# Optimization experiments

Measured on AMD Instinct MI355X. Metric: run time of the kernel, lower is better.

## Reference

```python
import jax, jax.numpy as jnp
import numpy as np

BATCH, TOK, DIM, OUT = 4, 2048, 4096, 4096
E, R, TOP_K = 8, 16, 2
SCALING = 16.0 / R  # lora_alpha / r


def setup_inputs() -> dict:
    key = jax.random.key(0)
    ks = jax.random.split(key, 6)
    return {
        "x": jax.random.normal(ks[0], (BATCH, TOK, DIM), dtype=jnp.float32),
        "W_base": jax.random.normal(ks[1], (OUT, DIM), dtype=jnp.float32) / np.sqrt(DIM),
        "b_base": jax.random.normal(ks[2], (OUT,), dtype=jnp.float32) * 0.01,
        "W_gate": jax.random.normal(ks[3], (E, DIM), dtype=jnp.float32) * 0.01,
        "A": jax.random.normal(ks[4], (E, R, DIM), dtype=jnp.float32) / np.sqrt(DIM),
        "B": jax.random.normal(ks[5], (OUT, OUT // OUT * R * 0 + R), dtype=jnp.float32)[None].repeat(E, 0) * 0.0 + jax.random.normal(ks[5], (E, OUT, R), dtype=jnp.float32) * 0.02,
    }


def reference(x, W_base, b_base, W_gate, A, B):
    # Base frozen linear: [B,N,D] @ [D,O] -> [B,N,O]
    result = jnp.einsum("bnd,od->bno", x, W_base) + b_base
    # Gating
    logits = jnp.einsum("bnd,ed->bne", x, W_gate)
    probs = jax.nn.softmax(logits.astype(jnp.float32), axis=-1)  # fp32 softmax
    top_p, top_i = jax.lax.top_k(probs, TOP_K)  # [B,N,K]
    top_p = top_p / jnp.sum(top_p, axis=-1, keepdims=True)  # top_k > 1 branch
    top_p = top_p.astype(x.dtype)
    # Scatter top-k probs back to dense [B,N,E] routing weights
    route_w = jnp.sum(jax.nn.one_hot(top_i, E, dtype=x.dtype) * top_p[..., None], axis=-2)
    # Per-expert LoRA: down-project all tokens for all experts (r is small),
    # weight by routing, then up-project and sum over experts.
    h = jnp.einsum("bnd,erd->bner", x, A)          # [B,N,E,r]
    hw = h * route_w[..., None]                      # mask/combine weighting
    delta = jnp.einsum("bner,eor->bno", hw, B)      # [B,N,O]
    return result + delta * SCALING
```

## Files before the change

kernel.cpp:

```cpp
#include <hip/hip_runtime.h>
#include <hip/hip_bf16.h>
#include <cstdint>

#define TOKENS 8192
#define DIM_   4096
#define OUTD   4096
#define NE     8
#define NR     16
#define LORA_COLS (NE*NR)
#define KCAT  (DIM_ + LORA_COLS)
#define NTILES (KCAT/64)
#define HSPLIT 8
#define HKC    (DIM_/HSPLIT)

typedef __attribute__((ext_vector_type(8))) short short8;
typedef __attribute__((ext_vector_type(4))) float f32x4;

__device__ __forceinline__ unsigned short f2bf(float f) {
  union { float f; unsigned u; } v; v.f = f;
  unsigned r = v.u + 0x7FFFu + ((v.u >> 16) & 1u);
  return (unsigned short)(r >> 16);
}

__device__ __forceinline__ void load_lds16(const void* g, void* l) {
  auto gp = reinterpret_cast<const __attribute__((address_space(1))) unsigned int*>(
      reinterpret_cast<uintptr_t>(g));
  auto lp = reinterpret_cast<__attribute__((address_space(3))) unsigned int*>(
      reinterpret_cast<uintptr_t>(l));
  __builtin_amdgcn_global_load_lds(gp, lp, 16, 0, 0);
}

#define BAR() asm volatile("s_barrier" ::: "memory")
#define LGKM0() do { asm volatile("s_waitcnt lgkmcnt(0)" ::: "memory"); \
                     __builtin_amdgcn_sched_barrier(0); } while (0)
#define VMW(N) asm volatile("s_waitcnt vmcnt(" #N ")" ::: "memory")

__global__ __launch_bounds__(256) void conv_w_kernel(
    const float* __restrict__ W, const float* __restrict__ Bm,
    const float* __restrict__ Am, unsigned short* __restrict__ Wcat,
    unsigned short* __restrict__ Acat, float scaling) {
  int b = blockIdx.x, tid = threadIdx.x;
  if (b < OUTD) {
    const float4* src = (const float4*)(W + (size_t)b * DIM_);
    unsigned short* dst = Wcat + (size_t)b * KCAT;
#pragma unroll
    for (int j = 0; j < DIM_ / 1024; ++j) {
      float4 v = src[j * 256 + tid];
      ushort4 o; o.x = f2bf(v.x); o.y = f2bf(v.y); o.z = f2bf(v.z); o.w = f2bf(v.w);
      *(ushort4*)(dst + (size_t)(j * 256 + tid) * 4) = o;
    }
    if (tid < LORA_COLS) {
      int e = tid >> 4, r = tid & 15;
      dst[DIM_ + tid] = f2bf(scaling * Bm[((size_t)e * OUTD + b) * NR + r]);
    }
  } else {
    int i = b - OUTD;
    const float4* src = (const float4*)(Am + (size_t)i * DIM_);
    unsigned short* dst = Acat + (size_t)i * DIM_;
#pragma unroll
    for (int j = 0; j < DIM_ / 1024; ++j) {
      float4 v = src[j * 256 + tid];
      ushort4 o; o.x = f2bf(v.x); o.y = f2bf(v.y); o.z = f2bf(v.z); o.w = f2bf(v.w);
      *(ushort4*)(dst + (size_t)(j * 256 + tid) * 4) = o;
    }
  }
}

__global__ __launch_bounds__(256) void prep_x_kernel(
    const float* __restrict__ x, const float* __restrict__ Wg,
    unsigned short* __restrict__ Xcat, int* __restrict__ ridx,
    float* __restrict__ rw) {
  __shared__ float red[32 * 257];
  __shared__ float lg[32];
  int tid = threadIdx.x;
  int t0 = blockIdx.x * 4;
  float acc[4][8];
#pragma unroll
  for (int ti = 0; ti < 4; ++ti)
#pragma unroll
    for (int e = 0; e < 8; ++e) acc[ti][e] = 0.f;
  const float4* x4 = (const float4*)x;
  const float4* wg4 = (const float4*)Wg;
#pragma unroll
  for (int j = 0; j < 4; ++j) {
    int dpos = j * 256 + tid;
    float4 wg[8];
#pragma unroll
    for (int e = 0; e < 8; ++e) wg[e] = wg4[e * 1024 + dpos];
#pragma unroll
    for (int ti = 0; ti < 4; ++ti) {
      float4 v = x4[(size_t)(t0 + ti) * 1024 + dpos];
      ushort4 o; o.x = f2bf(v.x); o.y = f2bf(v.y); o.z = f2bf(v.z); o.w = f2bf(v.w);
      *(ushort4*)&Xcat[(size_t)(t0 + ti) * KCAT + (size_t)dpos * 4] = o;
#pragma unroll
      for (int e = 0; e < 8; ++e)
        acc[ti][e] += v.x * wg[e].x + v.y * wg[e].y + v.z * wg[e].z + v.w * wg[e].w;
    }
  }
#pragma unroll
  for (int p = 0; p < 32; ++p) red[p * 257 + tid] = acc[p >> 3][p & 7];
  __syncthreads();
  {
    int p = tid >> 3, part = tid & 7;
    float s = 0.f;
#pragma unroll
    for (int i = 0; i < 32; ++i) s += red[p * 257 + part * 32 + i];
    s += __shfl_xor(s, 1);
    s += __shfl_xor(s, 2);
    s += __shfl_xor(s, 4);
    if (part == 0) lg[p] = s;
  }
  __syncthreads();
  if (tid < 4) {
    float l[8];
#pragma unroll
    for (int e = 0; e < 8; ++e) l[e] = lg[tid * 8 + e];
    int i0 = 0; float m0 = l[0];
#pragma unroll
    for (int e = 1; e < 8; ++e) if (l[e] > m0) { m0 = l[e]; i0 = e; }
    int i1 = -1; float m1 = -3.4e38f;
#pragma unroll
    for (int e = 0; e < 8; ++e) if (e != i0 && l[e] > m1) { m1 = l[e]; i1 = e; }
    float w0 = 1.0f / (1.0f + expf(m1 - m0));
    int t = t0 + tid;
    ridx[t * 2] = i0; ridx[t * 2 + 1] = i1;
    rw[t * 2] = w0;  rw[t * 2 + 1] = 1.0f - w0;
  }
}

template <int MODE>
__global__ __launch_bounds__(256) void gemm_kernel(
    const unsigned short* __restrict__ Aop, const unsigned short* __restrict__ Bop,
    float* __restrict__ Cout, unsigned short* __restrict__ CoutBf,
    const float* __restrict__ bias, const int* __restrict__ ridx,
    const float* __restrict__ rw,
    int M, int N, int K, int lda, int ldb, int ldc) {
  __shared__ __align__(16) unsigned short lsA[128 * 32];
  __shared__ __align__(16) unsigned short lsB[128 * 32];
  int tid = threadIdx.x;
  int lane = tid & 63, wave = tid >> 6;
  int wm = wave >> 1, wn = wave & 1;
  int row0 = blockIdx.x * 128, col0 = blockIdx.y * 128;

  f32x4 acc[4][4];
#pragma unroll
  for (int a = 0; a < 4; ++a)
#pragma unroll
    for (int b = 0; b < 4; ++b) acc[a][b] = (f32x4){0.f, 0.f, 0.f, 0.f};

  int lrow = lane >> 2;
  int lcol = (lane & 3) << 3;
  int fr = lane & 15, fk = (lane >> 4) << 3;

  const unsigned short* gA0 = Aop + (size_t)(row0 + wave * 32 + lrow) * lda + lcol;
  const unsigned short* gA1 = Aop + (size_t)(row0 + wave * 32 + 16 + lrow) * lda + lcol;
  const unsigned short* gB0 = Bop + (size_t)(col0 + wave * 32 + lrow) * ldb + lcol;
  const unsigned short* gB1 = Bop + (size_t)(col0 + wave * 32 + 16 + lrow) * ldb + lcol;

  for (int k0 = 0; k0 < K; k0 += 32) {
    load_lds16(gA0 + k0, lsA + wave * 1024);
    load_lds16(gA1 + k0, lsA + wave * 1024 + 512);
    load_lds16(gB0 + k0, lsB + wave * 1024);
    load_lds16(gB1 + k0, lsB + wave * 1024 + 512);
    __syncthreads();
    short8 af[4], bfr[4];
#pragma unroll
    for (int mi = 0; mi < 4; ++mi)
      af[mi] = *(const short8*)&lsA[(wm * 64 + mi * 16 + fr) * 32 + fk];
#pragma unroll
    for (int ni = 0; ni < 4; ++ni)
      bfr[ni] = *(const short8*)&lsB[(wn * 64 + ni * 16 + fr) * 32 + fk];
#pragma unroll
    for (int mi = 0; mi < 4; ++mi)
#pragma unroll
      for (int ni = 0; ni < 4; ++ni)
        acc[mi][ni] = __builtin_amdgcn_mfma_f32_16x16x32_bf16(af[mi], bfr[ni], acc[mi][ni], 0, 0, 0);
    __syncthreads();
  }

  int fg = lane >> 4;
  if (MODE == 0) {
#pragma unroll
    for (int ni = 0; ni < 4; ++ni) {
      int col = col0 + wn * 64 + ni * 16 + fr;
      float bv = bias[col];
#pragma unroll
      for (int mi = 0; mi < 4; ++mi)
#pragma unroll
        for (int j = 0; j < 4; ++j) {
          int row = row0 + wm * 64 + mi * 16 + fg * 4 + j;
          Cout[(size_t)row * ldc + col] = acc[mi][ni][j] + bv;
        }
    }
  } else {
#pragma unroll
    for (int mi = 0; mi < 4; ++mi)
#pragma unroll
      for (int j = 0; j < 4; ++j) {
        int row = row0 + wm * 64 + mi * 16 + fg * 4 + j;
        int i0 = ridx[row * 2], i1 = ridx[row * 2 + 1];
        float w0 = rw[row * 2], w1 = rw[row * 2 + 1];
#pragma unroll
        for (int ni = 0; ni < 4; ++ni) {
          int col = wn * 64 + ni * 16 + fr;
          int e = col >> 4;
          float w = (e == i0) ? w0 : ((e == i1) ? w1 : 0.f);
          CoutBf[(size_t)row * ldc + col] = f2bf(w * acc[mi][ni][j]);
        }
      }
  }
}

__global__ __launch_bounds__(256) void gemm_h_sk_kernel(
    const unsigned short* __restrict__ Aop,
    const unsigned short* __restrict__ Bop,
    float* __restrict__ Hpart) {
  __shared__ __align__(16) unsigned short lsA[128 * 32];
  __shared__ __align__(16) unsigned short lsB[128 * 32];
  int tid = threadIdx.x;
  int lane = tid & 63, wave = tid >> 6;
  int wm = wave >> 1, wn = wave & 1;
  int row0 = blockIdx.x * 128;
  int s = blockIdx.y;
  int kbeg = s * HKC;

  f32x4 acc[4][4];
#pragma unroll
  for (int a = 0; a < 4; ++a)
#pragma unroll
    for (int b = 0; b < 4; ++b) acc[a][b] = (f32x4){0.f, 0.f, 0.f, 0.f};

  int lrow = lane >> 2;
  int lcol = (lane & 3) << 3;
  int fr = lane & 15, fk = (lane >> 4) << 3;

  const unsigned short* gA0 = Aop + (size_t)(row0 + wave * 32 + lrow) * KCAT + lcol;
  const unsigned short* gA1 = Aop + (size_t)(row0 + wave * 32 + 16 + lrow) * KCAT + lcol;
  const unsigned short* gB0 = Bop + (size_t)(wave * 32 + lrow) * DIM_ + lcol;
  const unsigned short* gB1 = Bop + (size_t)(wave * 32 + 16 + lrow) * DIM_ + lcol;

  for (int k0 = kbeg; k0 < kbeg + HKC; k0 += 32) {
    load_lds16(gA0 + k0, lsA + wave * 1024);
    load_lds16(gA1 + k0, lsA + wave * 1024 + 512);
    load_lds16(gB0 + k0, lsB + wave * 1024);
    load_lds16(gB1 + k0, lsB + wave * 1024 + 512);
    __syncthreads();
    short8 af[4], bfr[4];
#pragma unroll
    for (int mi = 0; mi < 4; ++mi)
      af[mi] = *(const short8*)&lsA[(wm * 64 + mi * 16 + fr) * 32 + fk];
#pragma unroll
    for (int ni = 0; ni < 4; ++ni)
      bfr[ni] = *(const short8*)&lsB[(wn * 64 + ni * 16 + fr) * 32 + fk];
#pragma unroll
    for (int mi = 0; mi < 4; ++mi)
#pragma unroll
      for (int ni = 0; ni < 4; ++ni)
        acc[mi][ni] = __builtin_amdgcn_mfma_f32_16x16x32_bf16(af[mi], bfr[ni], acc[mi][ni], 0, 0, 0);
    __syncthreads();
  }

  int fg = lane >> 4;
  float* outp = Hpart + (size_t)s * TOKENS * 128;
#pragma unroll
  for (int ni = 0; ni < 4; ++ni) {
    int col = wn * 64 + ni * 16 + fr;
#pragma unroll
    for (int mi = 0; mi < 4; ++mi)
#pragma unroll
      for (int j = 0; j < 4; ++j) {
        int row = row0 + wm * 64 + mi * 16 + fg * 4 + j;
        outp[(size_t)row * 128 + col] = acc[mi][ni][j];
      }
  }
}

__global__ __launch_bounds__(256) void h_combine_kernel(
    const float* __restrict__ Hpart, const int* __restrict__ ridx,
    const float* __restrict__ rw, unsigned short* __restrict__ Xcat) {
  int gid = blockIdx.x * 256 + threadIdx.x;
  int t = gid >> 7, c = gid & 127;
  float s = 0.f;
#pragma unroll
  for (int i = 0; i < HSPLIT; ++i) s += Hpart[(size_t)i * TOKENS * 128 + gid];
  int e = c >> 4;
  int i0 = ridx[t * 2], i1 = ridx[t * 2 + 1];
  float w = (e == i0) ? rw[t * 2] : ((e == i1) ? rw[t * 2 + 1] : 0.f);
  Xcat[(size_t)t * KCAT + DIM_ + c] = f2bf(w * s);
}

#define RD_A4(dst, base, ks, mi0) do { \
  dst[0] = *(const short8*)((base) + (((mi0)+0)*2+(ks))*1024); \
  dst[1] = *(const short8*)((base) + (((mi0)+1)*2+(ks))*1024); \
  dst[2] = *(const short8*)((base) + (((mi0)+2)*2+(ks))*1024); \
  dst[3] = *(const short8*)((base) + (((mi0)+3)*2+(ks))*1024); } while (0)
#define RD_B4(dst, base, ks) do { \
  dst[0] = *(const short8*)((base) + 0*2048 + (ks)*1024); \
  dst[1] = *(const short8*)((base) + 1*2048 + (ks)*1024); \
  dst[2] = *(const short8*)((base) + 2*2048 + (ks)*1024); \
  dst[3] = *(const short8*)((base) + 3*2048 + (ks)*1024); } while (0)
#define MFMA_BLK(a4, b4, m0) do { \
  __builtin_amdgcn_s_setprio(1); \
  _Pragma("unroll") \
  for (int mi = 0; mi < 4; ++mi) { \
    _Pragma("unroll") \
    for (int ni = 0; ni < 4; ++ni) { \
      acc[(m0)+mi][ni] = __builtin_amdgcn_mfma_f32_16x16x32_bf16( \
          b4[ni], a4[mi], acc[(m0)+mi][ni], 0, 0, 0); } } \
  __builtin_amdgcn_s_setprio(0); } while (0)
#define STAGE(srcp, kofs, dst) do { \
  load_lds16((srcp) + (kofs), (dst)); \
  load_lds16((srcp) + (kofs) + 32, (dst) + 1024); } while (0)

__global__ __launch_bounds__(512, 2) void gemm256_kernel(
    const unsigned short* __restrict__ Aop,
    const unsigned short* __restrict__ Bop,
    float* __restrict__ Cout, const float* __restrict__ bias) {
  extern __shared__ char lds[];
  const int tid = threadIdx.x;
  const int lane = tid & 63, wave = tid >> 6;
  const int wm = wave >> 2, wn = wave & 3;
  const int fr = lane & 15, kg = lane >> 4;

  const int bid = blockIdx.x;
  const int swz = (bid & 7) * 64 + (bid >> 3);
  const int mt = swz >> 4, nt = swz & 15;
  const int row0 = mt * 256, col0 = nt * 256;

  const int srow = lane >> 2;
  const int scol = ((lane & 3) * 8) ^ (((lane >> 5) & 1) * 16);
  const unsigned short* sA0 = Aop + (size_t)(row0 +       wave * 16 + srow) * KCAT + scol;
  const unsigned short* sA1 = Aop + (size_t)(row0 + 128 + wave * 16 + srow) * KCAT + scol;
  const unsigned short* sB0 = Bop + (size_t)(col0 +       wave * 16 + srow) * KCAT + scol;
  const unsigned short* sB1 = Bop + (size_t)(col0 + 128 + wave * 16 + srow) * KCAT + scol;

  char* dA0b0 = lds +      0 + wave * 2048;
  char* dA1b0 = lds +  16384 + wave * 2048;
  char* dB0b0 = lds +  32768 + wave * 2048;
  char* dB1b0 = lds +  49152 + wave * 2048;
  char* dA0b1 = dA0b0 + 65536;
  char* dA1b1 = dA1b0 + 65536;
  char* dB0b1 = dB0b0 + 65536;
  char* dB1b1 = dB1b0 + 65536;

  const int swzo = (kg * 16) ^ ((fr >> 3) << 5);
  const char* rdA0 = lds + wm * 16384 + fr * 64 + swzo;
  const char* rdA1 = rdA0 + 65536;
  const char* rdB0 = lds + 32768 + (wn >> 1) * 16384 + (wn & 1) * 8192 + fr * 64 + swzo;
  const char* rdB1 = rdB0 + 65536;

  f32x4 acc[8][4];
#pragma unroll
  for (int a = 0; a < 8; ++a)
#pragma unroll
    for (int b = 0; b < 4; ++b) acc[a][b] = (f32x4){0.f, 0.f, 0.f, 0.f};

  STAGE(sA0, 0, dA0b0); STAGE(sA1, 0, dA1b0);
  STAGE(sB0, 0, dB0b0); STAGE(sB1, 0, dB1b0);
  STAGE(sB0, 64, dB0b1); STAGE(sA0, 64, dA0b1);
  VMW(4);
  BAR();

  for (int i = 0; i < NTILES / 2 - 1; ++i) {
    const int k1 = (2 * i + 1) * 64, k2 = k1 + 64, k3 = k1 + 128;
    short8 aL[4], aH[4], a1L[4], a1H[4], b0f[4], b1f[4];
    RD_A4(aL, rdA0, 0, 0); RD_B4(b0f, rdB0, 0);
    STAGE(sB1, k1, dB1b1);
    BAR(); LGKM0();
    MFMA_BLK(aL, b0f, 0);
    BAR();
    RD_A4(aH, rdA0, 0, 4); RD_B4(b1f, rdB0, 1);
    STAGE(sA1, k1, dA1b1);
    BAR(); LGKM0();
    MFMA_BLK(aH, b0f, 4);
    BAR();
    RD_A4(a1L, rdA0, 1, 0); RD_A4(a1H, rdA0, 1, 4);
    STAGE(sB0, k2, dB0b0);
    BAR(); LGKM0();
    MFMA_BLK(a1L, b1f, 0);
    BAR();
    STAGE(sA0, k2, dA0b0);
    BAR();
    MFMA_BLK(a1H, b1f, 4);
    VMW(4);
    BAR();
    RD_A4(aL, rdA1, 0, 0); RD_B4(b0f, rdB1, 0);
    STAGE(sB1, k2, dB1b0);
    BAR(); LGKM0();
    MFMA_BLK(aL, b0f, 0);
    BAR();
    RD_A4(aH, rdA1, 0, 4); RD_B4(b1f, rdB1, 1);
    STAGE(sA1, k2, dA1b0);
    BAR(); LGKM0();
    MFMA_BLK(aH, b0f, 4);
    BAR();
    RD_A4(a1L, rdA1, 1, 0); RD_A4(a1H, rdA1, 1, 4);
    STAGE(sB0, k3, dB0b1);
    BAR(); LGKM0();
    MFMA_BLK(a1L, b1f, 0);
    BAR();
    STAGE(sA0, k3, dA0b1);
    BAR();
    MFMA_BLK(a1H, b1f, 4);
    VMW(4);
    BAR();
  }

  {
    const int k65 = 65 * 64;
    short8 aL[4], aH[4], a1L[4], a1H[4], b0f[4], b1f[4];
    RD_A4(aL, rdA0, 0, 0); RD_B4(b0f, rdB0, 0);
    STAGE(sB1, k65, dB1b1);
    BAR(); LGKM0();
    MFMA_BLK(aL, b0f, 0);
    BAR();
    RD_A4(aH, rdA0, 0, 4); RD_B4(b1f, rdB0, 1);
    STAGE(sA1, k65, dA1b1);
    BAR(); LGKM0();
    MFMA_BLK(aH, b0f, 4);
    BAR();
    RD_A4(a1L, rdA0, 1, 0); RD_A4(a1H, rdA0, 1, 4);
    BAR(); LGKM0();
    MFMA_BLK(a1L, b1f, 0);
    BAR();
    MFMA_BLK(a1H, b1f, 4);
    VMW(0);
    BAR();
    RD_A4(aL, rdA1, 0, 0); RD_B4(b0f, rdB1, 0); RD_A4(aH, rdA1, 0, 4);
    LGKM0();
    MFMA_BLK(aL, b0f, 0);
    MFMA_BLK(aH, b0f, 4);
    RD_A4(a1L, rdA1, 1, 0); RD_B4(b1f, rdB1, 1); RD_A4(a1H, rdA1, 1, 4);
    LGKM0();
    MFMA_BLK(a1L, b1f, 0);
    MFMA_BLK(a1H, b1f, 4);
  }

#pragma unroll
  for (int ni = 0; ni < 4; ++ni) {
    int colb = col0 + wn * 64 + ni * 16 + kg * 4;
    float4 bv = *(const float4*)&bias[colb];
#pragma unroll
    for (int mi = 0; mi < 8; ++mi) {
      int row = row0 + wm * 128 + mi * 16 + fr;
      float4 v;
      v.x = acc[mi][ni][0] + bv.x;
      v.y = acc[mi][ni][1] + bv.y;
      v.z = acc[mi][ni][2] + bv.z;
      v.w = acc[mi][ni][3] + bv.w;
      *(float4*)&Cout[(size_t)row * OUTD + colb] = v;
    }
  }
}

extern "C" void kernel_launch(void* const* d_in, const int* in_sizes, int n_in,
                              void* d_out, int out_size, void* d_ws, size_t ws_size,
                              hipStream_t stream) {
  const float* x  = (const float*)d_in[0];
  const float* Wb = (const float*)d_in[1];
  const float* bb = (const float*)d_in[2];
  const float* Wg = (const float*)d_in[3];
  const float* Am = (const float*)d_in[4];
  const float* Bm = (const float*)d_in[5];
  float* out = (float*)d_out;

  unsigned short* Wcat = (unsigned short*)d_ws;
  unsigned short* Xcat = Wcat + (size_t)OUTD * KCAT;
  unsigned short* Acat = Xcat + (size_t)TOKENS * KCAT;
  int*   ridx = (int*)(Acat + (size_t)LORA_COLS * DIM_);
  float* rw   = (float*)(ridx + (size_t)TOKENS * 2);
  float* Hpart = (float*)(rw + (size_t)TOKENS * 2);

  const size_t ws_needed = (size_t)((char*)(Hpart + (size_t)HSPLIT * TOKENS * 128)
                                    - (char*)d_ws);
  const bool use_splitk = (ws_size >= ws_needed);

  const float scaling = 16.0f / (float)NR;

  hipFuncSetAttribute((const void*)gemm256_kernel,
                      hipFuncAttributeMaxDynamicSharedMemorySize, 131072);

  conv_w_kernel<<<dim3(OUTD + LORA_COLS), dim3(256), 0, stream>>>(
      Wb, Bm, Am, Wcat, Acat, scaling);
  prep_x_kernel<<<dim3(TOKENS / 4), dim3(256), 0, stream>>>(
      x, Wg, Xcat, ridx, rw);
  if (use_splitk) {
    gemm_h_sk_kernel<<<dim3(TOKENS / 128, HSPLIT), dim3(256), 0, stream>>>(
        Xcat, Acat, Hpart);
    h_combine_kernel<<<dim3(TOKENS * 128 / 256), dim3(256), 0, stream>>>(
        Hpart, ridx, rw, Xcat);
  } else {
    gemm_kernel<1><<<dim3(TOKENS / 128, 1), dim3(256), 0, stream>>>(
        Xcat, Acat, (float*)nullptr, Xcat + DIM_, (const float*)nullptr,
        ridx, rw, TOKENS, LORA_COLS, DIM_, KCAT, DIM_, KCAT);
  }
  gemm256_kernel<<<dim3(512), dim3(512), 131072, stream>>>(Xcat, Wcat, out, bb);
}
```

Baseline: 323.9 us.

## Software-pipeline LDS fragment reads one MFMA block ahead with partial lgkmcnt waits

Restructures the GEMM main loop so that LDS fragment reads for the next MFMA block are issued before the current block's MFMAs. It replaces full lgkmcnt(0) waits with partial waits (lgkmcnt 8/4), so LDS latency overlaps with matrix math. The fragment registers are hoisted out of the loop and carried across iterations, with a prologue read and a reworked epilogue. This raises register pressure, and wrong wait counts could cause stale-data hazards.

```diff
diff --git a/kernel.cpp b/kernel.cpp
--- a/kernel.cpp
+++ b/kernel.cpp
@@ -31,7 +31,7 @@
 }
 
 #define BAR() asm volatile("s_barrier" ::: "memory")
-#define LGKM0() do { asm volatile("s_waitcnt lgkmcnt(0)" ::: "memory"); \
+#define LGKM(N) do { asm volatile("s_waitcnt lgkmcnt(" #N ")" ::: "memory"); \
                      __builtin_amdgcn_sched_barrier(0); } while (0)
 #define VMW(N) asm volatile("s_waitcnt vmcnt(" #N ")" ::: "memory")
 
@@ -355,84 +355,95 @@
 #pragma unroll
     for (int b = 0; b < 4; ++b) acc[a][b] = (f32x4){0.f, 0.f, 0.f, 0.f};
 
+  short8 aL[4], aH[4], a1L[4], a1H[4], b0f[4], b1f[4];
+
   STAGE(sA0, 0, dA0b0); STAGE(sA1, 0, dA1b0);
   STAGE(sB0, 0, dB0b0); STAGE(sB1, 0, dB1b0);
   STAGE(sB0, 64, dB0b1); STAGE(sA0, 64, dA0b1);
   VMW(4);
   BAR();
+  RD_A4(aL, rdA0, 0, 0); RD_B4(b0f, rdB0, 0);
 
   for (int i = 0; i < NTILES / 2 - 1; ++i) {
     const int k1 = (2 * i + 1) * 64, k2 = k1 + 64, k3 = k1 + 128;
-    short8 aL[4], aH[4], a1L[4], a1H[4], b0f[4], b1f[4];
+    RD_A4(aH, rdA0, 0, 4); RD_B4(b1f, rdB0, 1);
+    STAGE(sB1, k1, dB1b1);
+    BAR(); LGKM(8);
+    MFMA_BLK(aL, b0f, 0);
+    BAR();
+    RD_A4(a1L, rdA0, 1, 0);
+    STAGE(sA1, k1, dA1b1);
+    BAR(); LGKM(4);
+    MFMA_BLK(aH, b0f, 4);
+    BAR();
+    RD_A4(a1H, rdA0, 1, 4);
+    STAGE(sB0, k2, dB0b0);
+    BAR(); LGKM(4);
+    MFMA_BLK(a1L, b1f, 0);
+    BAR();
+    STAGE(sA0, k2, dA0b0);
+    VMW(4);
+    BAR();
+    RD_A4(aL, rdA1, 0, 0); RD_B4(b0f, rdB1, 0);
+    LGKM(8);
+    MFMA_BLK(a1H, b1f, 4);
+    BAR();
+    RD_A4(aH, rdA1, 0, 4); RD_B4(b1f, rdB1, 1);
+    STAGE(sB1, k2, dB1b0);
+    BAR(); LGKM(8);
+    MFMA_BLK(aL, b0f, 0);
+    BAR();
+    RD_A4(a1L, rdA1, 1, 0);
+    STAGE(sA1, k2, dA1b0);
+    BAR(); LGKM(4);
+    MFMA_BLK(aH, b0f, 4);
+    BAR();
+    RD_A4(a1H, rdA1, 1, 4);
+    STAGE(sB0, k3, dB0b1);
+    BAR(); LGKM(4);
+    MFMA_BLK(a1L, b1f, 0);
+    BAR();
+    STAGE(sA0, k3, dA0b1);
+    VMW(4);
+    BAR();
     RD_A4(aL, rdA0, 0, 0); RD_B4(b0f, rdB0, 0);
-    STAGE(sB1, k1, dB1b1);
-    BAR(); LGKM0();
-    MFMA_BLK(aL, b0f, 0);
-    BAR();
-    RD_A4(aH, rdA0, 0, 4); RD_B4(b1f, rdB0, 1);
-    STAGE(sA1, k1, dA1b1);
-    BAR(); LGKM0();
-    MFMA_BLK(aH, b0f, 4);
-    BAR();
-    RD_A4(a1L, rdA0, 1, 0); RD_A4(a1H, rdA0, 1, 4);
-    STAGE(sB0, k2, dB0b0);
-    BAR(); LGKM0();
-    MFMA_BLK(a1L, b1f, 0);
-    BAR();
-    STAGE(sA0, k2, dA0b0);
-    BAR();
+    LGKM(8);
     MFMA_BLK(a1H, b1f, 4);
-    VMW(4);
-    BAR();
-    RD_A4(aL, rdA1, 0, 0); RD_B4(b0f, rdB1, 0);
-    STAGE(sB1, k2, dB1b0);
-    BAR(); LGKM0();
-    MFMA_BLK(aL, b0f, 0);
-    BAR();
-    RD_A4(aH, rdA1, 0, 4); RD_B4(b1f, rdB1, 1);
-    STAGE(sA1, k2, dA1b0);
-    BAR(); LGKM0();
-    MFMA_BLK(aH, b0f, 4);
-    BAR();
-    RD_A4(a1L, rdA1, 1, 0); RD_A4(a1H, rdA1, 1, 4);
-    STAGE(sB0, k3, dB0b1);
-    BAR(); LGKM0();
-    MFMA_BLK(a1L, b1f, 0);
-    BAR();
-    STAGE(sA0, k3, dA0b1);
-    BAR();
-    MFMA_BLK(a1H, b1f, 4);
-    VMW(4);
     BAR();
   }
 
   {
     const int k65 = 65 * 64;
-    short8 aL[4], aH[4], a1L[4], a1H[4], b0f[4], b1f[4];
-    RD_A4(aL, rdA0, 0, 0); RD_B4(b0f, rdB0, 0);
+    RD_A4(aH, rdA0, 0, 4); RD_B4(b1f, rdB0, 1);
     STAGE(sB1, k65, dB1b1);
-    BAR(); LGKM0();
+    BAR(); LGKM(8);
     MFMA_BLK(aL, b0f, 0);
     BAR();
-    RD_A4(aH, rdA0, 0, 4); RD_B4(b1f, rdB0, 1);
+    RD_A4(a1L, rdA0, 1, 0);
     STAGE(sA1, k65, dA1b1);
-    BAR(); LGKM0();
+    BAR(); LGKM(4);
     MFMA_BLK(aH, b0f, 4);
     BAR();
-    RD_A4(a1L, rdA0, 1, 0); RD_A4(a1H, rdA0, 1, 4);
-    BAR(); LGKM0();
+    RD_A4(a1H, rdA0, 1, 4);
+    BAR(); LGKM(4);
     MFMA_BLK(a1L, b1f, 0);
     BAR();
+    VMW(0);
+    BAR();
+    RD_A4(aL, rdA1, 0, 0); RD_B4(b0f, rdB1, 0);
+    LGKM(8);
     MFMA_BLK(a1H, b1f, 4);
-    VMW(0);
-    BAR();
-    RD_A4(aL, rdA1, 0, 0); RD_B4(b0f, rdB1, 0); RD_A4(aH, rdA1, 0, 4);
-    LGKM0();
+    BAR();
+    RD_A4(aH, rdA1, 0, 4); RD_B4(b1f, rdB1, 1);
+    LGKM(8);
     MFMA_BLK(aL, b0f, 0);
+    RD_A4(a1L, rdA1, 1, 0);
+    LGKM(4);
     MFMA_BLK(aH, b0f, 4);
-    RD_A4(a1L, rdA1, 1, 0); RD_B4(b1f, rdB1, 1); RD_A4(a1H, rdA1, 1, 4);
-    LGKM0();
+    RD_A4(a1H, rdA1, 1, 4);
+    LGKM(4);
     MFMA_BLK(a1L, b1f, 0);
+    LGKM(0);
     MFMA_BLK(a1H, b1f, 4);
   }
 
```

New measurement: 319.8 us. About the same (-1.2%).
